# Performance work log

Measured on AMD Instinct MI355X. Metric: run time of the kernel, lower is better.

The kernel has to match this reference:

```python
import jax, jax.numpy as jnp
import numpy as np

HIDDEN = 768
HEADS = 12
HEAD_DIM = HIDDEN // HEADS
NORM = float(np.sqrt(HIDDEN))  # module divides by sqrt(hidden_size), not sqrt(head_dim)


def setup_inputs() -> dict:
    key = jax.random.key(0)
    ks = jax.random.split(key, 7)
    B, S, H = 8, 1024, HIDDEN
    scale = 0.02
    return {
        "hidden_states": jax.random.normal(ks[0], (B, S, H), dtype=jnp.float32),
        "Wq": jax.random.normal(ks[1], (H, H), dtype=jnp.float32) * scale,
        "bq": jax.random.normal(ks[2], (H,), dtype=jnp.float32) * scale,
        "Wk": jax.random.normal(ks[3], (H, H), dtype=jnp.float32) * scale,
        "bk": jax.random.normal(ks[4], (H,), dtype=jnp.float32) * scale,
        "Wv": jax.random.normal(ks[5], (H, H), dtype=jnp.float32) * scale,
        "bv": jax.random.normal(ks[6], (H,), dtype=jnp.float32) * scale,
    }


def reference(hidden_states, Wq, bq, Wk, bk, Wv, bv):
    B, S, H = hidden_states.shape
    def heads(x):  # [B,S,H] -> [B,nh,S,hd]
        return x.reshape(B, S, HEADS, HEAD_DIM).transpose(0, 2, 1, 3)
    q = heads(hidden_states @ Wq + bq)
    k = heads(hidden_states @ Wk + bk)
    v = heads(hidden_states @ Wv + bv)
    # naive quadratic attention (world_size=1 ring): scores materialized
    scores = jnp.einsum("bhqd,bhkd->bhqk", q, k) / NORM
    probs = jax.nn.softmax(scores, axis=-1)  # dropout prob = 0.0
    ctx = jnp.einsum("bhqk,bhkd->bhqd", probs, v)
    # [B,nh,S,hd] -> [B,S,H]
    return ctx.transpose(0, 2, 1, 3).reshape(B, S, H)
```

## Files before the change

kernel.cpp:

```cpp
#include <hip/hip_runtime.h>
#include <hip/hip_bf16.h>
#include <stdint.h>

typedef __attribute__((ext_vector_type(8))) short short8;
typedef __attribute__((ext_vector_type(4))) float f32x4;
typedef __attribute__((ext_vector_type(4))) unsigned short u16x4;

#define HIDDEN 768
#define HEADS 12
#define HD 64
#define NB 8
#define SEQ 1024
#define MTOT (NB*SEQ)
#define INV_NORM 0.03608439182435161f

typedef const __attribute__((address_space(1))) uint32_t* gas1_t;
typedef __attribute__((address_space(3))) uint32_t* las3_t;
#define GL_LDS16(g, l) __builtin_amdgcn_global_load_lds((gas1_t)(g), (las3_t)(l), 16, 0, 0)

static __device__ __forceinline__ unsigned short f2bf(float f){
  uint32_t u = __builtin_bit_cast(uint32_t, f);
  u += 0x7fffu + ((u >> 16) & 1u);
  return (unsigned short)(u >> 16);
}
static __device__ __forceinline__ unsigned short f2bf_hw(float f){
  return __builtin_bit_cast(unsigned short, __float2bfloat16(f));
}

#define DPP_STEP(x, ctrl, OP) { \
  int _t = __builtin_amdgcn_update_dpp(0, __builtin_bit_cast(int,(x)), (ctrl), 0xf, 0xf, true); \
  (x) = OP((x), __builtin_bit_cast(float,_t)); }
static __device__ __forceinline__ float addf(float a, float b){ return a+b; }
static __device__ __forceinline__ float dpp_sum16(float x){
  DPP_STEP(x, 0xB1, addf)
  DPP_STEP(x, 0x4E, addf)
  DPP_STEP(x, 0x141, addf)
  DPP_STEP(x, 0x140, addf)
  return x;
}

__global__ void convert_x_kernel(const float* __restrict__ x, unsigned short* __restrict__ xb){
  int i = blockIdx.x * 256 + threadIdx.x;
  float4 v = reinterpret_cast<const float4*>(x)[i];
  u16x4 o;
  o[0]=f2bf(v.x); o[1]=f2bf(v.y); o[2]=f2bf(v.z); o[3]=f2bf(v.w);
  reinterpret_cast<u16x4*>(xb)[i] = o;
}

__global__ void transpose_w_kernel(const float* __restrict__ Wq, const float* __restrict__ Wk,
                                   const float* __restrict__ Wv, unsigned short* __restrict__ Wt){
  __shared__ float t[32][33];
  int z = blockIdx.z;
  const float* W = (z==0) ? Wq : ((z==1) ? Wk : Wv);
  unsigned short* o = Wt + (size_t)z * HIDDEN * HIDDEN;
  int n0 = blockIdx.x * 32, k0 = blockIdx.y * 32;
  int x = threadIdx.x & 31, y0 = threadIdx.x >> 5;
#pragma unroll
  for(int p=0;p<4;p++){ int y = y0 + p*8; t[y][x] = W[(size_t)(k0+y)*HIDDEN + n0 + x]; }
  __syncthreads();
#pragma unroll
  for(int p=0;p<4;p++){ int y = y0 + p*8; o[(size_t)(n0+y)*HIDDEN + k0 + x] = f2bf(t[x][y]); }
}

__global__ __launch_bounds__(256, 4) void gemm_qkv_kernel(
    const unsigned short* __restrict__ Xb, const unsigned short* __restrict__ Wt,
    const float* __restrict__ bq, const float* __restrict__ bk, const float* __restrict__ bv,
    unsigned short* __restrict__ Qg, unsigned short* __restrict__ Kg, unsigned short* __restrict__ Vg)
{
  __shared__ alignas(16) unsigned short lA[128*64];
  __shared__ alignas(16) unsigned short lB[128*64];
  int wgid = blockIdx.x;
  int xcd = wgid & 7, idx = wgid >> 3;
  int y = xcd + 8*(idx/18);
  int within = idx % 18;
  int xb = within % 6, z = within / 6;
  const unsigned short* W = Wt + (size_t)z*HIDDEN*HIDDEN;
  const float* bias = (z==0) ? bq : ((z==1) ? bk : bv);
  unsigned short* out = (z==0) ? Qg : ((z==1) ? Kg : Vg);
  int m0 = y * 128, n0 = xb * 128;
  int tid = threadIdx.x;
  int w = tid >> 6, lane = tid & 63, l16 = lane & 15, g = lane >> 4;
  int wm = w >> 1, wn = w & 1;
  f32x4 acc[4][4] = {};
  for(int kt=0; kt<HIDDEN; kt+=64){
    __syncthreads();
#pragma unroll
    for(int p=0;p<4;p++){
      int t2 = p*256 + tid;
      int r = t2 >> 3;
      int cb = (((t2 & 7) << 4) ^ ((r & 7) << 4));
      GL_LDS16(Xb + (size_t)(m0 + r)*HIDDEN + kt + (cb >> 1), lA + p*2048 + w*512);
      GL_LDS16(W  + (size_t)(n0 + r)*HIDDEN + kt + (cb >> 1), lB + p*2048 + w*512);
    }
    __syncthreads();
#pragma unroll
    for(int kk=0;kk<2;kk++){
      short8 af[4], bf[4];
#pragma unroll
      for(int i=0;i<4;i++){
        int row = wm*64 + i*16 + l16;
        af[i] = *reinterpret_cast<const short8*>(
            reinterpret_cast<const unsigned char*>(lA) + row*128 + ((kk*64 + g*16) ^ ((row&7)<<4)));
      }
#pragma unroll
      for(int j=0;j<4;j++){
        int row = wn*64 + j*16 + l16;
        bf[j] = *reinterpret_cast<const short8*>(
            reinterpret_cast<const unsigned char*>(lB) + row*128 + ((kk*64 + g*16) ^ ((row&7)<<4)));
      }
#pragma unroll
      for(int i=0;i<4;i++)
#pragma unroll
        for(int j=0;j<4;j++)
          acc[i][j] = __builtin_amdgcn_mfma_f32_16x16x32_bf16(af[i], bf[j], acc[i][j], 0, 0, 0);
    }
  }
#pragma unroll
  for(int i=0;i<4;i++){
    int mb = m0 + wm*64 + i*16 + g*4;
#pragma unroll
    for(int j=0;j<4;j++){
      int n = n0 + wn*64 + j*16 + l16;
      float bi = bias[n];
      int h = n >> 6, d = n & 63;
#pragma unroll
      for(int r=0;r<4;r++){
        int m = mb + r;
        int b = m >> 10, s = m & 1023;
        float cv = acc[i][j][r] + bi;
        if(z == 0) cv *= INV_NORM;
        out[((size_t)(b*HEADS + h)*SEQ + s)*HD + d] = f2bf(cv);
      }
    }
  }
}

__global__ void transpose_v_kernel(const unsigned short* __restrict__ Vg, unsigned short* __restrict__ Vt){
  __shared__ alignas(16) unsigned short t[64][72];
  int bh = blockIdx.y;
  int s0 = blockIdx.x * 64;
  int tid = threadIdx.x;
  int s = tid >> 2, dq = (tid & 3) * 16;
  const unsigned short* src = Vg + ((size_t)bh*SEQ + s0 + s)*HD + dq;
  short8 v0 = *reinterpret_cast<const short8*>(src);
  short8 v1 = *reinterpret_cast<const short8*>(src + 8);
#pragma unroll
  for(int e=0;e<8;e++){ t[dq+e][s] = (unsigned short)v0[e]; t[dq+8+e][s] = (unsigned short)v1[e]; }
  __syncthreads();
  int d = tid >> 2, sq = (tid & 3) * 16;
  unsigned short* dst = Vt + ((size_t)bh*HD + d)*SEQ + s0 + sq;
  *reinterpret_cast<short8*>(dst)     = *reinterpret_cast<const short8*>(&t[d][sq]);
  *reinterpret_cast<short8*>(dst + 8) = *reinterpret_cast<const short8*>(&t[d][sq + 8]);
}

__global__ __launch_bounds__(256, 3) void attn_kernel(
    const unsigned short* __restrict__ Qg, const unsigned short* __restrict__ Kg,
    const unsigned short* __restrict__ Vt, float* __restrict__ out)
{
  __shared__ alignas(16) unsigned short lK[2][64*64];
  __shared__ alignas(16) unsigned short lV[2][64*64];
  __shared__ alignas(16) unsigned short lP[4*16*72];
  int wgid = blockIdx.x;
  int xcd = wgid & 7, ix = wgid >> 3;
  int bh = xcd*12 + (ix >> 3), qb = ix & 7;
  int b = bh / HEADS, h = bh % HEADS;
  int tid = threadIdx.x, w = tid >> 6, lane = tid & 63, l16 = lane & 15, g = lane >> 4;

  const unsigned short* Qbase = Qg + ((size_t)bh*SEQ + qb*128 + w*32)*HD;
  short8 qA0 = *reinterpret_cast<const short8*>(Qbase + l16*HD + g*8);
  short8 qA1 = *reinterpret_cast<const short8*>(Qbase + l16*HD + 32 + g*8);
  short8 qB0 = *reinterpret_cast<const short8*>(Qbase + (16+l16)*HD + g*8);
  short8 qB1 = *reinterpret_cast<const short8*>(Qbase + (16+l16)*HD + 32 + g*8);

  unsigned short* Pw = lP + w*(16*72);
  f32x4 oacc[2][4] = {};
  float lpart[2][4] = {};

#define STAGE(buf, kt) do { \
    int k0s = (kt)*64; \
    _Pragma("unroll") \
    for(int p=0;p<2;p++){ \
      int t2 = p*256 + tid; \
      int r = t2 >> 3; \
      int cb = (((t2 & 7) << 4) ^ ((r & 7) << 4)); \
      GL_LDS16(Kg + ((size_t)bh*SEQ + k0s + r)*HD + (cb >> 1), &lK[buf][0] + p*2048 + w*512); \
      GL_LDS16(Vt + ((size_t)bh*HD + r)*SEQ + k0s + (cb >> 1), &lV[buf][0] + p*2048 + w*512); \
    } \
  } while(0)

  STAGE(0, 0);
  __syncthreads();

  for(int kt=0; kt<SEQ/64; kt++){
    int cur = kt & 1;
    if(kt+1 < SEQ/64) STAGE(cur^1, kt+1);

    short8 kf[4][2], vf[4][2];
#pragma unroll
    for(int j=0;j<4;j++){
      int row = j*16 + l16;
      int sw = (row & 7) << 4;
      const unsigned char* kbase = reinterpret_cast<const unsigned char*>(&lK[cur][0]) + row*128;
      const unsigned char* vbase = reinterpret_cast<const unsigned char*>(&lV[cur][0]) + row*128;
      kf[j][0] = *reinterpret_cast<const short8*>(kbase + ((g*16) ^ sw));
      kf[j][1] = *reinterpret_cast<const short8*>(kbase + ((64 + g*16) ^ sw));
      vf[j][0] = *reinterpret_cast<const short8*>(vbase + ((g*16) ^ sw));
      vf[j][1] = *reinterpret_cast<const short8*>(vbase + ((64 + g*16) ^ sw));
    }

#pragma unroll
    for(int rg=0; rg<2; rg++){
      short8 q0 = rg ? qB0 : qA0;
      short8 q1 = rg ? qB1 : qA1;
      f32x4 sacc[4];
#pragma unroll
      for(int j=0;j<4;j++){
        f32x4 zz = {};
        zz      = __builtin_amdgcn_mfma_f32_16x16x32_bf16(q0, kf[j][0], zz, 0,0,0);
        sacc[j] = __builtin_amdgcn_mfma_f32_16x16x32_bf16(q1, kf[j][1], zz, 0,0,0);
      }
      float pv[4][4];
#pragma unroll
      for(int r=0;r<4;r++){
#pragma unroll
        for(int j=0;j<4;j++) pv[j][r] = __expf(sacc[j][r]);
        lpart[rg][r] += (pv[0][r] + pv[1][r]) + (pv[2][r] + pv[3][r]);
      }
#pragma unroll
      for(int r=0;r<4;r++){
        int prow = g*4 + r;
#pragma unroll
        for(int j=0;j<4;j++) Pw[prow*72 + j*16 + l16] = f2bf_hw(pv[j][r]);
      }
      asm volatile("s_waitcnt lgkmcnt(0)" ::: "memory");
      short8 pa0 = *reinterpret_cast<const short8*>(Pw + l16*72 + g*8);
      short8 pa1 = *reinterpret_cast<const short8*>(Pw + l16*72 + 32 + g*8);
#pragma unroll
      for(int jn=0;jn<4;jn++){
        oacc[rg][jn] = __builtin_amdgcn_mfma_f32_16x16x32_bf16(pa0, vf[jn][0], oacc[rg][jn], 0,0,0);
        oacc[rg][jn] = __builtin_amdgcn_mfma_f32_16x16x32_bf16(pa1, vf[jn][1], oacc[rg][jn], 0,0,0);
      }
    }
    __syncthreads();
  }

#pragma unroll
  for(int rg=0;rg<2;rg++)
#pragma unroll
  for(int r=0;r<4;r++){
    int s = qb*128 + w*32 + rg*16 + g*4 + r;
    float invl = 1.0f / dpp_sum16(lpart[rg][r]);
    float* orow = out + ((size_t)b*SEQ + s)*HIDDEN + h*HD;
#pragma unroll
    for(int jn=0;jn<4;jn++) orow[jn*16 + l16] = oacc[rg][jn][r] * invl;
  }
#undef STAGE
}

extern "C" void kernel_launch(void* const* d_in, const int* in_sizes, int n_in,
                              void* d_out, int out_size, void* d_ws, size_t ws_size,
                              hipStream_t stream) {
  const float* hs = (const float*)d_in[0];
  const float* Wq = (const float*)d_in[1];
  const float* bq = (const float*)d_in[2];
  const float* Wk = (const float*)d_in[3];
  const float* bk = (const float*)d_in[4];
  const float* Wv = (const float*)d_in[5];
  const float* bv = (const float*)d_in[6];
  float* out = (float*)d_out;

  char* ws = (char*)d_ws;
  unsigned short* Xb = (unsigned short*)ws;
  unsigned short* Wt = (unsigned short*)(ws + (size_t)12582912);
  unsigned short* Qg = (unsigned short*)(ws + (size_t)16121856);
  unsigned short* Kg = Qg + (size_t)MTOT*HIDDEN;
  unsigned short* Vg = Kg + (size_t)MTOT*HIDDEN;
  unsigned short* Vt = Vg + (size_t)MTOT*HIDDEN;

  convert_x_kernel<<<MTOT*HIDDEN/4/256, 256, 0, stream>>>(hs, Xb);
  transpose_w_kernel<<<dim3(24,24,3), 256, 0, stream>>>(Wq, Wk, Wv, Wt);
  gemm_qkv_kernel<<<1152, 256, 0, stream>>>(Xb, Wt, bq, bk, bv, Qg, Kg, Vg);
  transpose_v_kernel<<<dim3(16,96), 256, 0, stream>>>(Vg, Vt);
  attn_kernel<<<768, 256, 0, stream>>>(Qg, Kg, Vt, out);
}
```

Before: 100.1 us.

## Fuse V transpose into QKV GEMM epilogue, use exp2 and batch P staging

The QKV GEMM epilogue now writes V directly in transposed [bh, d, s] layout with packed 4-element stores, which removes the separate transpose_v kernel and its extra pass over V. Q is pre-scaled by log2(e)/sqrt(hidden) so the softmax can use the hardware exp2 instead of __expf. In the attention loop both row groups' score MFMAs run before either exp step, and P is staged into separate LDS slices per row group with a single wait, giving more overlap at the cost of doubled P shared memory. Softmax still has no max subtraction, so it relies on scores staying small.

```diff
diff --git a/kernel.cpp b/kernel.cpp
--- a/kernel.cpp
+++ b/kernel.cpp
@@ -12,7 +12,7 @@
 #define NB 8
 #define SEQ 1024
 #define MTOT (NB*SEQ)
-#define INV_NORM 0.03608439182435161f
+#define QSCALE 0.05205887314427834f
 
 typedef const __attribute__((address_space(1))) uint32_t* gas1_t;
 typedef __attribute__((address_space(3))) uint32_t* las3_t;
@@ -25,6 +25,13 @@
 }
 static __device__ __forceinline__ unsigned short f2bf_hw(float f){
   return __builtin_bit_cast(unsigned short, __float2bfloat16(f));
+}
+static __device__ __forceinline__ float fexp2(float x){
+#if __has_builtin(__builtin_amdgcn_exp2f)
+  return __builtin_amdgcn_exp2f(x);
+#else
+  return exp2f(x);
+#endif
 }
 
 #define DPP_STEP(x, ctrl, OP) { \
@@ -65,7 +72,7 @@
 __global__ __launch_bounds__(256, 4) void gemm_qkv_kernel(
     const unsigned short* __restrict__ Xb, const unsigned short* __restrict__ Wt,
     const float* __restrict__ bq, const float* __restrict__ bk, const float* __restrict__ bv,
-    unsigned short* __restrict__ Qg, unsigned short* __restrict__ Kg, unsigned short* __restrict__ Vg)
+    unsigned short* __restrict__ Qg, unsigned short* __restrict__ Kg, unsigned short* __restrict__ Vt)
 {
   __shared__ alignas(16) unsigned short lA[128*64];
   __shared__ alignas(16) unsigned short lB[128*64];
@@ -76,7 +83,6 @@
   int xb = within % 6, z = within / 6;
   const unsigned short* W = Wt + (size_t)z*HIDDEN*HIDDEN;
   const float* bias = (z==0) ? bq : ((z==1) ? bk : bv);
-  unsigned short* out = (z==0) ? Qg : ((z==1) ? Kg : Vg);
   int m0 = y * 128, n0 = xb * 128;
   int tid = threadIdx.x;
   int w = tid >> 6, lane = tid & 63, l16 = lane & 15, g = lane >> 4;
@@ -115,42 +121,43 @@
           acc[i][j] = __builtin_amdgcn_mfma_f32_16x16x32_bf16(af[i], bf[j], acc[i][j], 0, 0, 0);
     }
   }
-#pragma unroll
-  for(int i=0;i<4;i++){
-    int mb = m0 + wm*64 + i*16 + g*4;
-#pragma unroll
-    for(int j=0;j<4;j++){
-      int n = n0 + wn*64 + j*16 + l16;
-      float bi = bias[n];
-      int h = n >> 6, d = n & 63;
-#pragma unroll
-      for(int r=0;r<4;r++){
-        int m = mb + r;
-        int b = m >> 10, s = m & 1023;
-        float cv = acc[i][j][r] + bi;
-        if(z == 0) cv *= INV_NORM;
-        out[((size_t)(b*HEADS + h)*SEQ + s)*HD + d] = f2bf(cv);
-      }
-    }
-  }
-}
-
-__global__ void transpose_v_kernel(const unsigned short* __restrict__ Vg, unsigned short* __restrict__ Vt){
-  __shared__ alignas(16) unsigned short t[64][72];
-  int bh = blockIdx.y;
-  int s0 = blockIdx.x * 64;
-  int tid = threadIdx.x;
-  int s = tid >> 2, dq = (tid & 3) * 16;
-  const unsigned short* src = Vg + ((size_t)bh*SEQ + s0 + s)*HD + dq;
-  short8 v0 = *reinterpret_cast<const short8*>(src);
-  short8 v1 = *reinterpret_cast<const short8*>(src + 8);
-#pragma unroll
-  for(int e=0;e<8;e++){ t[dq+e][s] = (unsigned short)v0[e]; t[dq+8+e][s] = (unsigned short)v1[e]; }
-  __syncthreads();
-  int d = tid >> 2, sq = (tid & 3) * 16;
-  unsigned short* dst = Vt + ((size_t)bh*HD + d)*SEQ + s0 + sq;
-  *reinterpret_cast<short8*>(dst)     = *reinterpret_cast<const short8*>(&t[d][sq]);
-  *reinterpret_cast<short8*>(dst + 8) = *reinterpret_cast<const short8*>(&t[d][sq + 8]);
+  if(z == 2){
+#pragma unroll
+    for(int i=0;i<4;i++){
+      int mb = m0 + wm*64 + i*16 + g*4;
+      int b = mb >> 10, s = mb & 1023;
+#pragma unroll
+      for(int j=0;j<4;j++){
+        int n = n0 + wn*64 + j*16 + l16;
+        float bi = bias[n];
+        int h = n >> 6, d = n & 63;
+        u16x4 pk;
+#pragma unroll
+        for(int r=0;r<4;r++) pk[r] = f2bf(acc[i][j][r] + bi);
+        *reinterpret_cast<u16x4*>(Vt + ((size_t)(b*HEADS + h)*HD + d)*SEQ + s) = pk;
+      }
+    }
+  } else {
+    unsigned short* out = (z==0) ? Qg : Kg;
+#pragma unroll
+    for(int i=0;i<4;i++){
+      int mb = m0 + wm*64 + i*16 + g*4;
+#pragma unroll
+      for(int j=0;j<4;j++){
+        int n = n0 + wn*64 + j*16 + l16;
+        float bi = bias[n];
+        int h = n >> 6, d = n & 63;
+#pragma unroll
+        for(int r=0;r<4;r++){
+          int m = mb + r;
+          int b = m >> 10, s = m & 1023;
+          float cv = acc[i][j][r] + bi;
+          if(z == 0) cv *= QSCALE;
+          out[((size_t)(b*HEADS + h)*SEQ + s)*HD + d] = f2bf(cv);
+        }
+      }
+    }
+  }
 }
 
 __global__ __launch_bounds__(256, 3) void attn_kernel(
@@ -159,7 +166,7 @@
 {
   __shared__ alignas(16) unsigned short lK[2][64*64];
   __shared__ alignas(16) unsigned short lV[2][64*64];
-  __shared__ alignas(16) unsigned short lP[4*16*72];
+  __shared__ alignas(16) unsigned short lP[8*16*72];
   int wgid = blockIdx.x;
   int xcd = wgid & 7, ix = wgid >> 3;
   int bh = xcd*12 + (ix >> 3), qb = ix & 7;
@@ -172,7 +179,6 @@
   short8 qB0 = *reinterpret_cast<const short8*>(Qbase + (16+l16)*HD + g*8);
   short8 qB1 = *reinterpret_cast<const short8*>(Qbase + (16+l16)*HD + 32 + g*8);
 
-  unsigned short* Pw = lP + w*(16*72);
   f32x4 oacc[2][4] = {};
   float lpart[2][4] = {};
 
@@ -208,22 +214,26 @@
       vf[j][1] = *reinterpret_cast<const short8*>(vbase + ((64 + g*16) ^ sw));
     }
 
+    f32x4 sacc[2][4];
 #pragma unroll
     for(int rg=0; rg<2; rg++){
       short8 q0 = rg ? qB0 : qA0;
       short8 q1 = rg ? qB1 : qA1;
-      f32x4 sacc[4];
 #pragma unroll
       for(int j=0;j<4;j++){
         f32x4 zz = {};
-        zz      = __builtin_amdgcn_mfma_f32_16x16x32_bf16(q0, kf[j][0], zz, 0,0,0);
-        sacc[j] = __builtin_amdgcn_mfma_f32_16x16x32_bf16(q1, kf[j][1], zz, 0,0,0);
-      }
+        zz           = __builtin_amdgcn_mfma_f32_16x16x32_bf16(q0, kf[j][0], zz, 0,0,0);
+        sacc[rg][j]  = __builtin_amdgcn_mfma_f32_16x16x32_bf16(q1, kf[j][1], zz, 0,0,0);
+      }
+    }
+#pragma unroll
+    for(int rg=0; rg<2; rg++){
+      unsigned short* Pw = lP + (w*2+rg)*(16*72);
       float pv[4][4];
 #pragma unroll
       for(int r=0;r<4;r++){
 #pragma unroll
-        for(int j=0;j<4;j++) pv[j][r] = __expf(sacc[j][r]);
+        for(int j=0;j<4;j++) pv[j][r] = fexp2(sacc[rg][j][r]);
         lpart[rg][r] += (pv[0][r] + pv[1][r]) + (pv[2][r] + pv[3][r]);
       }
 #pragma unroll
@@ -232,7 +242,11 @@
 #pragma unroll
         for(int j=0;j<4;j++) Pw[prow*72 + j*16 + l16] = f2bf_hw(pv[j][r]);
       }
-      asm volatile("s_waitcnt lgkmcnt(0)" ::: "memory");
+    }
+    asm volatile("s_waitcnt lgkmcnt(0)" ::: "memory");
+#pragma unroll
+    for(int rg=0; rg<2; rg++){
+      const unsigned short* Pw = lP + (w*2+rg)*(16*72);
       short8 pa0 = *reinterpret_cast<const short8*>(Pw + l16*72 + g*8);
       short8 pa1 = *reinterpret_cast<const short8*>(Pw + l16*72 + 32 + g*8);
 #pragma unroll
@@ -274,12 +288,10 @@
   unsigned short* Wt = (unsigned short*)(ws + (size_t)12582912);
   unsigned short* Qg = (unsigned short*)(ws + (size_t)16121856);
   unsigned short* Kg = Qg + (size_t)MTOT*HIDDEN;
-  unsigned short* Vg = Kg + (size_t)MTOT*HIDDEN;
-  unsigned short* Vt = Vg + (size_t)MTOT*HIDDEN;
+  unsigned short* Vt = Kg + (size_t)MTOT*HIDDEN;
 
   convert_x_kernel<<<MTOT*HIDDEN/4/256, 256, 0, stream>>>(hs, Xb);
   transpose_w_kernel<<<dim3(24,24,3), 256, 0, stream>>>(Wq, Wk, Wv, Wt);
-  gemm_qkv_kernel<<<1152, 256, 0, stream>>>(Xb, Wt, bq, bk, bv, Qg, Kg, Vg);
-  transpose_v_kernel<<<dim3(16,96), 256, 0, stream>>>(Vg, Vt);
+  gemm_qkv_kernel<<<1152, 256, 0, stream>>>(Xb, Wt, bq, bk, bv, Qg, Kg, Vt);
   attn_kernel<<<768, 256, 0, stream>>>(Qg, Kg, Vt, out);
 }
```

After: 94.28 us. -5.8%, faster.
